# Optimization experiments

Measured on AMD Instinct MI355X. Metric: run time of the kernel, lower is better.

## Reference

```python
import jax, jax.numpy as jnp
import numpy as np

MAX_RADIUS = 3.0
NUM_BASIS = 8
NUM_NEIGHBORS = 16.0
N, E, NS, NV, B, D, T, L, HR = 2048, 32768, 32, 16, 8, 32, 32, 2, 64
NW = NS * 2 * NV + NV * 2 * (NS + NV) + NV * 2 * NV  # 3072 per-edge TP weights


def smooth_cutoff(x):
    u = 2.0 * (x - 1.0)
    y = 0.5 * (1.0 - jnp.cos(jnp.pi * u))
    y = jnp.where(u > 0, 0.0, y)
    y = jnp.where(u < -1, 1.0, y)
    return y


def bessel_basis(length):
    # soft_one_hot_linspace(basis='bessel', cutoff=False) * sqrt(NUM_BASIS)
    k = jnp.arange(1, NUM_BASIS + 1, dtype=length.dtype) * jnp.pi
    l = jnp.maximum(length, 1e-9)[..., None]
    return jnp.sqrt(2.0 / MAX_RADIUS) * jnp.sin(k * l / MAX_RADIUS) / l * np.sqrt(NUM_BASIS)


def get_edge_info(x, edge_src, edge_dst):
    n = x.shape[0]
    xr = x.reshape(n, 2, 3)                         # 2 vectors per node
    vec = xr[edge_src] - xr[edge_dst]               # [E,2,3]
    length = jnp.sqrt(jnp.sum(vec * vec, axis=-1) + 1e-12)   # [E,2]
    sh = np.sqrt(3.0) * vec / length[..., None]     # component-normalized l=1 SH
    feat = bessel_basis(length)                     # [E,2,B]
    attr = smooth_cutoff(length / MAX_RADIUS)[..., None] * sh  # [E,2,3]
    return feat.reshape(vec.shape[0], -1), attr


def setup_inputs() -> dict:
    key = jax.random.key(0)
    ks = jax.random.split(key, 20)
    inp = {
        'x': jax.random.normal(ks[0], (N, 6), jnp.float32),
        'batch': jnp.zeros((N,), jnp.int64 if jax.config.jax_enable_x64 else jnp.int32),
        'node_attr': jax.random.randint(ks[1], (N,), 0, T),
        'edge_src': jax.random.randint(ks[2], (E,), 0, N),
        'edge_dst': jax.random.randint(ks[3], (E,), 0, N),
        'emb': jax.random.normal(ks[4], (T, D), jnp.float32),
        'W_uplift': jax.random.normal(ks[5], (NV, 2), jnp.float32),
        'W_sc_s': jax.random.normal(ks[6], (L, NS, D, NS + NV), jnp.float32),
        'W_sc_v': jax.random.normal(ks[7], (L, NV, D, NV), jnp.float32),
        'W_l1_s': jax.random.normal(ks[8], (L, NS, NS), jnp.float32),
        'W_l1_v': jax.random.normal(ks[9], (L, NV, NV), jnp.float32),
        'W_r1': jax.random.normal(ks[10], (L, 2 * B, HR), jnp.float32),
        'W_r2': jax.random.normal(ks[11], (L, HR, NW), jnp.float32),
        'W_l2_s': jax.random.normal(ks[12], (L, NS + NV, NS + NV), jnp.float32),
        'W_l2_v': jax.random.normal(ks[13], (L, NV, NV), jnp.float32),
        'W_si_s': jax.random.normal(ks[14], (L, NS, NS), jnp.float32),
        'W_si_v': jax.random.normal(ks[15], (L, NV, NV), jnp.float32),
        'h': jnp.ones((L,), jnp.float32) * 0.01,
        'mix': jnp.ones((L,), jnp.float32) * 0.5,
    }
    return inp


def reference(x, batch, node_attr, edge_src, edge_dst, emb, W_uplift, W_sc_s, W_sc_v,
              W_l1_s, W_l1_v, W_r1, W_r2, W_l2_s, W_l2_v, W_si_s, W_si_v, h, mix):
    n = x.shape[0]
    a = emb[node_attr]                              # node attr embedding [N,D]
    Q, _ = jnp.linalg.qr(W_uplift)                  # semi-unitary uplift [NV,2]
    y_v = jnp.einsum('ci,nik->nck', Q, x.reshape(n, 2, 3))   # uplift vectors
    y_s = jnp.zeros((n, NS), x.dtype)
    y, y_old = (y_s, y_v), (y_s, y_v)
    n1 = NS * 2 * NV
    n2 = NV * 2 * (NS + NV)
    for i in range(L):
        ef, ea = get_edge_info(x, edge_src, edge_dst)       # [E,2B], [E,2,3]
        ys, yv = y
        # self-connection tensor product (features x node_attr)
        sc_s = jnp.einsum('ni,na,iaj->nj', ys, a, W_sc_s[i]) / np.sqrt(NS * D)
        sc_v = jnp.einsum('nck,na,caj->njk', yv, a, W_sc_v[i]) / np.sqrt(NV * D)
        # lin1
        s1 = ys @ W_l1_s[i] / np.sqrt(NS)
        v1 = jnp.einsum('nck,cj->njk', yv, W_l1_v[i]) / np.sqrt(NV)
        # radial MLP -> per-edge TP weights
        hr = jax.nn.silu(ef @ W_r1[i] / np.sqrt(2 * B))
        w = hr @ W_r2[i] / np.sqrt(HR)                       # [E,NW]
        w_sv = w[:, :n1].reshape(E, NS, 2, NV)
        w_vs = w[:, n1:n1 + n2].reshape(E, NV, 2, NS + NV)
        w_vv = w[:, n1 + n2:].reshape(E, NV, 2, NV)
        s_src, v_src = s1[edge_src], v1[edge_src]
        # edge tensor product: 0e x 1o -> 1o, 1o x 1o -> 0e (dot), 1o x 1o -> 1o (cross)
        e_v = jnp.einsum('esmj,es,emk->ejk', w_sv, s_src, ea) / np.sqrt(NS * 2)
        dots = jnp.einsum('eck,emk->ecm', v_src, ea)
        e_s = jnp.einsum('ecmj,ecm->ej', w_vs, dots) / np.sqrt(NV * 2 * 3)
        crs = jnp.cross(v_src[:, :, None, :], ea[:, None, :, :])  # [E,NV,2,3]
        e_v = e_v + jnp.einsum('ecmj,ecmk->ejk', w_vv, crs) / np.sqrt(NV * 2 * 2)
        # scatter-aggregate over destination nodes
        ns_ = jax.ops.segment_sum(e_s, edge_dst, num_segments=n) / np.sqrt(NUM_NEIGHBORS)
        nv_ = jax.ops.segment_sum(e_v, edge_dst, num_segments=n) / np.sqrt(NUM_NEIGHBORS)
        s2 = ns_ @ W_l2_s[i] / np.sqrt(NS + NV)
        v2 = jnp.einsum('nck,cj->njk', nv_, W_l2_v[i]) / np.sqrt(NV)
        conv_s, conv_v = sc_s + s2, sc_v + v2
        # gate
        g_s = jax.nn.silu(conv_s[:, :NS])
        g_v = jax.nn.sigmoid(conv_s[:, NS:])[:, :, None] * conv_v
        # self-interaction
        si_s = ys @ W_si_s[i] / np.sqrt(NS)
        si_v = jnp.einsum('nck,cj->njk', yv, W_si_v[i]) / np.sqrt(NV)
        # gated leapfrog update
        h2, m = h[i] ** 2, mix[i]
        new_s = 2 * ys - y_old[0] + h2 * (m * g_s + (m - 1) * si_s)
        new_v = 2 * yv - y_old[1] + h2 * (m * g_v + (m - 1) * si_v)
        y_old, y = y, (new_s, new_v)
        x = jnp.einsum('ci,nck->nik', Q, y[1]).reshape(n, 6)  # project back
    return x
```

## Files before the change

kernel.cpp:

```cpp
#include <hip/hip_runtime.h>
#include <hip/hip_bf16.h>
#include <math.h>

#define NN   2048
#define EE   32768
#define NS   32
#define NV   16
#define NB   8
#define DD   32
#define TT   32
#define LL   2
#define HRD  64
#define NWW  3072
#define TPE  128
#define PI_F 3.14159265358979323846f

#define SC_SCS (1.0f/32.0f)
#define SC_SCV 0.04419417382415922f
#define SC_L1S 0.17677669529663687f
#define SC_L1V 0.25f
#define SC_R1  0.25f
#define SC_R2  0.125f
#define SC_ES  0.10206207261596575f
#define SC_EV  0.125f
#define SC_AGG 0.25f
#define SC_L2S 0.14433756729740643f
#define SC_L2V 0.25f
#define SC_SIS 0.17677669529663687f
#define SC_SIV 0.25f

typedef __attribute__((ext_vector_type(8))) short  short8;
typedef __attribute__((ext_vector_type(4))) float  floatx4;

__device__ __forceinline__ floatx4 mfma16(short8 a, short8 b, floatx4 c) {
    return __builtin_amdgcn_mfma_f32_16x16x32_bf16(a, b, c, 0, 0, 0);
}

__device__ __forceinline__ void seg_reduce_store(
        const float (*red)[49], const int* dst_s,
        const int* __restrict__ row_ptr, int ebase,
        int tid, int wave, int lane,
        int* segstart_s, int* wtot_s, int* nseg_s,
        float* __restrict__ outg) {
    int seg_flag = 0, seg_lidx = 0;
    if (tid < TPE) {
        seg_flag = (tid == 0) || (dst_s[tid] != dst_s[tid - 1]);
        unsigned long long m = __ballot(seg_flag != 0);
        if (lane == 0) wtot_s[wave] = (int)__popcll(m);
        seg_lidx = (int)__popcll(m & ((1ull << lane) - 1ull));
    }
    __syncthreads();
    if (seg_flag) segstart_s[seg_lidx + (wave ? wtot_s[0] : 0)] = tid;
    if (tid == 0) {
        int ns = wtot_s[0] + wtot_s[1];
        nseg_s[0] = ns;
        segstart_s[ns] = TPE;
    }
    __syncthreads();
    int nseg = nseg_s[0];
    for (int w = tid; w < nseg * 48; w += 256) {
        int seg = w / 48, c = w - seg * 48;
        int p0 = segstart_s[seg], p1 = segstart_s[seg + 1];
        int d = dst_s[p0];
        float run = 0.f;
        for (int pos = p0; pos < p1; ++pos) run += red[pos][c];
        if (row_ptr[d] >= ebase && row_ptr[d + 1] <= ebase + TPE)
            outg[d * 48 + c] = run;
        else
            atomicAdd(&outg[d * 48 + c], run);
    }
}

__global__ void k_setup(const float* __restrict__ Wup, float* __restrict__ Q,
                        const float* __restrict__ emb,
                        const float* __restrict__ Wscs, const float* __restrict__ Wscv,
                        float* __restrict__ WtS, float* __restrict__ WtV,
                        const float* __restrict__ Wr2, __hip_bfloat16* __restrict__ wr2t,
                        int* __restrict__ deg, int* __restrict__ cursor) {
    int b = blockIdx.x;
    if (b == 0) {
        if (threadIdx.x != 0) return;
        double A[16][2], tau[2];
        for (int i = 0; i < 16; ++i)
            for (int j = 0; j < 2; ++j) A[i][j] = (double)Wup[i*2 + j];
        for (int j = 0; j < 2; ++j) {
            double alpha = A[j][j];
            double xn2 = 0.0;
            for (int i = j + 1; i < 16; ++i) xn2 += A[i][j]*A[i][j];
            if (xn2 == 0.0) {
                tau[j] = 0.0;
            } else {
                double nrm  = sqrt(alpha*alpha + xn2);
                double beta = (alpha >= 0.0) ? -nrm : nrm;
                tau[j] = (beta - alpha) / beta;
                double s = 1.0 / (alpha - beta);
                for (int i = j + 1; i < 16; ++i) A[i][j] *= s;
                A[j][j] = beta;
            }
            for (int k = j + 1; k < 2; ++k) {
                double w = A[j][k];
                for (int i = j + 1; i < 16; ++i) w += A[i][j]*A[i][k];
                w *= tau[j];
                A[j][k] -= w;
                for (int i = j + 1; i < 16; ++i) A[i][k] -= A[i][j]*w;
            }
        }
        double Qm[16][2];
        for (int i = 0; i < 16; ++i)
            for (int j = 0; j < 2; ++j) Qm[i][j] = (i == j) ? 1.0 : 0.0;
        for (int j = 1; j >= 0; --j) {
            for (int k = 0; k < 2; ++k) {
                double w = Qm[j][k];
                for (int i = j + 1; i < 16; ++i) w += A[i][j]*Qm[i][k];
                w *= tau[j];
                Qm[j][k] -= w;
                for (int i = j + 1; i < 16; ++i) Qm[i][k] -= A[i][j]*w;
            }
        }
        for (int i = 0; i < 16; ++i)
            for (int j = 0; j < 2; ++j) Q[i*2 + j] = (float)Qm[i][j];
    } else if (b <= 64) {
        int lt = b - 1;
        int l = lt >> 5, t = lt & 31;
        __shared__ float es[32];
        if (threadIdx.x < 32) es[threadIdx.x] = emb[t*DD + threadIdx.x];
        __syncthreads();
        const float* Ws = Wscs + (size_t)l*NS*DD*48;
        float* oS = WtS + (size_t)(l*TT + t)*NS*48;
        for (int idx = threadIdx.x; idx < NS*48; idx += 256) {
            int i = idx / 48, j = idx % 48;
            float acc = 0.f;
            for (int a = 0; a < 32; ++a) acc += es[a]*Ws[(i*DD + a)*48 + j];
            oS[idx] = acc;
        }
        const float* Wv = Wscv + (size_t)l*NV*DD*NV;
        float* oV = WtV + (size_t)(l*TT + t)*NV*NV;
        for (int idx = threadIdx.x; idx < NV*NV; idx += 256) {
            int c = idx / 16, j = idx % 16;
            float acc = 0.f;
            for (int a = 0; a < 32; ++a) acc += es[a]*Wv[(c*DD + a)*NV + j];
            oV[idx] = acc;
        }
    } else if (b <= 1600) {
        int idx = (b - 65)*256 + threadIdx.x;
        int l = idx / (HRD*NWW);
        int r = idx - l*(HRD*NWW);
        int k = r / NWW;
        int c = r - k*NWW;
        int ch = c >> 6, cc = c & 63, q = cc >> 4, tcc = cc & 15;
        int h = k >> 5, qd = (k >> 3) & 3, j = k & 7;
        size_t dst = (size_t)l*(NWW*HRD)
                   + (size_t)((ch*32 + q*8 + h*4 + qd)*128 + tcc*8 + j);
        wr2t[dst] = __float2bfloat16(Wr2[idx]);
    } else {
        int i = (b - 1601)*256 + threadIdx.x;
        if (i < NN) { deg[i] = 0; cursor[i] = 0; }
    }
}

__global__ void k_hist(const int* __restrict__ edst, int* __restrict__ deg) {
    int e = blockIdx.x*256 + threadIdx.x;
    atomicAdd(&deg[edst[e]], 1);
}

__global__ void k_scan(const int* __restrict__ deg, int* __restrict__ row_ptr) {
    __shared__ int wsum[4];
    int t = threadIdx.x;
    int lane = t & 63, wave = t >> 6;
    int loc[8]; int s = 0;
    for (int k = 0; k < 8; ++k) { loc[k] = deg[t*8 + k]; s += loc[k]; }
    int inc = s;
    for (int d = 1; d < 64; d <<= 1) {
        int v = __shfl_up(inc, d);
        if (lane >= d) inc += v;
    }
    if (lane == 63) wsum[wave] = inc;
    __syncthreads();
    int woff = 0;
    for (int w = 0; w < wave; ++w) woff += wsum[w];
    int off = woff + inc - s;
    for (int k = 0; k < 8; ++k) { row_ptr[t*8 + k] = off; off += loc[k]; }
    if (t == 255) row_ptr[2048] = off;
}

__global__ void k_fill(const int* __restrict__ esrc, const int* __restrict__ edst,
                       const int* __restrict__ row_ptr, int* __restrict__ cursor,
                       int* __restrict__ srcs, int* __restrict__ dsts,
                       const float* __restrict__ xin, const float* __restrict__ Q,
                       float* __restrict__ ys0, float* __restrict__ yv0,
                       float* __restrict__ ys1, float* __restrict__ yv1,
                       float* __restrict__ xcur,
                       const float* __restrict__ Wl1v0,
                       float* __restrict__ s1, float* __restrict__ v1,
                       float* __restrict__ nsb, float* __restrict__ nsb2,
                       float* __restrict__ nvba, float* __restrict__ nvbb) {
    if (blockIdx.x < 128) {
        int e = blockIdx.x*256 + threadIdx.x;
        int d = edst[e];
        int pos = atomicAdd(&cursor[d], 1);
        int p = row_ptr[d] + pos;
        srcs[p] = esrc[e];
        dsts[p] = d;
    } else {
        int idx = (blockIdx.x - 128)*256 + threadIdx.x;
        int n = idx / 48, r = idx - 48*(idx / 48);
        int j = r/3, k = r - 3*j;
        float xk  = xin[n*6 + k];
        float xk3 = xin[n*6 + 3 + k];
        float yvv = Q[j*2 + 0]*xk + Q[j*2 + 1]*xk3;
        yv0[idx] = yvv;
        yv1[idx] = yvv;
        float a = 0.f;
        for (int c = 0; c < 16; ++c) {
            float yc = Q[c*2 + 0]*xk + Q[c*2 + 1]*xk3;
            a += yc*Wl1v0[c*16 + j];
        }
        v1[idx] = a*SC_L1V;
        nsb[idx] = 0.f; nsb2[idx] = 0.f;
        nvba[idx] = 0.f; nvbb[idx] = 0.f;
        if (r < 32) {
            int si = n*32 + r;
            ys0[si] = 0.f; ys1[si] = 0.f; s1[si] = 0.f;
        }
        if (r < 6) xcur[n*6 + r] = xin[n*6 + r];
    }
}

__global__ void __launch_bounds__(256, 3) k_tp(
        const float* __restrict__ xcur,
        const int* __restrict__ srcs, const int* __restrict__ dsts,
        const int* __restrict__ row_ptr,
        const float* __restrict__ Wr1l,
        const __hip_bfloat16* __restrict__ wr2tl,
        const float* __restrict__ s1g, const float* __restrict__ v1g,
        float* __restrict__ nsb, float* __restrict__ nsb2,
        float* __restrict__ nvba, float* __restrict__ nvbb) {
    __shared__ __align__(16) char smem[31680];
    __shared__ float ea_s[TPE][9];
    __shared__ int   src_s[TPE];
    __shared__ int   dst_s[TPE];
    __shared__ int   segstart_s[TPE + 1];
    __shared__ int   wtot_s[2];
    __shared__ int   nseg_s[1];

    int bid = blockIdx.x;
    int region = bid % 3;
    int tile   = bid / 3;
    int ebase  = tile*TPE;
    int tid = threadIdx.x;
    int wave = tid >> 6, lane = tid & 63;
    int tc = tid & 15;
    int quad = lane >> 4;

    float* ef_lds  = (float*)smem;
    float* Wr1_lds = (float*)(smem + 8448);
    __hip_bfloat16* hr_lds = (__hip_bfloat16*)(smem + 12544);

    if (tid < TPE) { src_s[tid] = srcs[ebase + tid]; dst_s[tid] = dsts[ebase + tid]; }
    for (int i = tid; i < 16*64; i += 256) Wr1_lds[i] = Wr1l[i];

    if (tid < TPE) {
        int s = src_s[tid], d = dst_s[tid];
        for (int m = 0; m < 2; ++m) {
            float v0 = xcur[s*6 + m*3 + 0] - xcur[d*6 + m*3 + 0];
            float v1_ = xcur[s*6 + m*3 + 1] - xcur[d*6 + m*3 + 1];
            float v2 = xcur[s*6 + m*3 + 2] - xcur[d*6 + m*3 + 2];
            float len = sqrtf(v0*v0 + v1_*v1_ + v2*v2 + 1e-12f);
            float inv = 1.0f/len;
            float theta = len*(PI_F/3.0f);
            float s1v = sinf(theta), c1v = cosf(theta);
            float sc  = 2.3094010767585034f*inv;
            float sp = 0.f, scur = s1v, twoc = 2.f*c1v;
            for (int bq = 0; bq < 8; ++bq) {
                ef_lds[(m*8 + bq)*132 + tid] = sc*scur;
                float sn = twoc*scur - sp;
                sp = scur; scur = sn;
            }
            float u = 2.0f*(len*(1.0f/3.0f) - 1.0f);
            float cut;
            if (u > 0.f) cut = 0.f;
            else if (u < -1.f) cut = 1.f;
            else cut = 0.5f*(1.0f - cosf(PI_F*u));
            float shs = 1.7320508075688772f*inv*cut;
            ea_s[tid][m*3 + 0] = shs*v0;
            ea_s[tid][m*3 + 1] = shs*v1_;
            ea_s[tid][m*3 + 2] = shs*v2;
        }
    }
    __syncthreads();

    {
        int e = tid >> 1, h = tid & 1;
        float z[32];
        #pragma unroll
        for (int k = 0; k < 32; ++k) z[k] = 0.f;
        for (int f = 0; f < 16; ++f) {
            float efv = ef_lds[f*132 + e];
            #pragma unroll
            for (int k = 0; k < 32; ++k) z[k] += efv*Wr1_lds[f*64 + h*32 + k];
        }
        #pragma unroll
        for (int q8 = 0; q8 < 4; ++q8) {
            __hip_bfloat16 tmp[8];
            #pragma unroll
            for (int j = 0; j < 8; ++j) {
                float zz = z[q8*8 + j]*SC_R1;
                tmp[j] = __float2bfloat16(zz/(1.0f + expf(-zz)));
            }
            *(short8*)&hr_lds[e*72 + h*32 + q8*8] = *(short8*)tmp;
        }
    }
    __syncthreads();

    const short* hrp = (const short*)(smem + 12544);
    short8 a_lo[2], a_hi[2];
    #pragma unroll
    for (int rt = 0; rt < 2; ++rt) {
        int row = (wave*2 + rt)*16 + tc;
        a_lo[rt] = *(const short8*)(hrp + row*72 + quad*8);
        a_hi[rt] = *(const short8*)(hrp + row*72 + 32 + quad*8);
    }
    __syncthreads();

    const char* wb = (const char*)wr2tl;
    const float sES = SC_R2*SC_ES*SC_AGG;
    const float sEV = SC_R2*SC_EV*SC_AGG;

    if (region == 0) {
        float (*s1t)[132] = (float(*)[132])smem;
        for (int i = tid; i < TPE*32; i += 256) {
            int e = i >> 5, s = i & 31;
            s1t[s][e] = s1g[src_s[e]*32 + s];
        }
        __syncthreads();

        float accF[2][4][2] = {};
        for (int ci = 0; ci < 16; ++ci) {
            const char* Bc = wb + (size_t)ci*8192 + lane*16;
            #pragma unroll
            for (int q = 0; q < 4; ++q) {
                short8 b_lo = *(const short8*)(Bc + q*2048);
                short8 b_hi = *(const short8*)(Bc + q*2048 + 1024);
                floatx4 c0 = {0.f,0.f,0.f,0.f}, c1 = {0.f,0.f,0.f,0.f};
                c0 = mfma16(a_lo[0], b_lo, c0); c0 = mfma16(a_hi[0], b_hi, c0);
                c1 = mfma16(a_lo[1], b_lo, c1); c1 = mfma16(a_hi[1], b_hi, c1);
                int m = q & 1;
                int sidx = ci*2 + (q >> 1);
                #pragma unroll
                for (int rt = 0; rt < 2; ++rt) {
                    int e0r = (wave*2 + rt)*16 + quad*4;
                    float4 sv = *(const float4*)&s1t[sidx][e0r];
                    floatx4 cc = rt ? c1 : c0;
                    #pragma unroll
                    for (int i = 0; i < 4; ++i)
                        accF[rt][i][m] += cc[i]*((&sv.x)[i]);
                }
            }
        }
        __syncthreads();
        float (*red)[49] = (float(*)[49])smem;
        #pragma unroll
        for (int rt = 0; rt < 2; ++rt) {
            int e0r = (wave*2 + rt)*16 + quad*4;
            #pragma unroll
            for (int i = 0; i < 4; ++i) {
                int pos = e0r + i;
                float f0 = accF[rt][i][0]*sEV, f1 = accF[rt][i][1]*sEV;
                #pragma unroll
                for (int k = 0; k < 3; ++k)
                    red[pos][tc*3 + k] = f0*ea_s[pos][k] + f1*ea_s[pos][3 + k];
            }
        }
        __syncthreads();
        seg_reduce_store((const float(*)[49])smem, dst_s, row_ptr, ebase,
                         tid, wave, lane, segstart_s, wtot_s, nseg_s, nvba);
    } else if (region == 1) {
        float (*dots_t)[132] = (float(*)[132])smem;
        float (*v1h)[132]    = (float(*)[132])(smem + 16896);
        for (int half = 0; half < 2; ++half) {
            int jbase = half*24;
            for (int i = tid; i < TPE*24; i += 256) {
                int e = i/24, j = i - 24*(i/24);
                v1h[j][e] = v1g[src_s[e]*48 + jbase + j];
            }
            __syncthreads();
            for (int i = tid; i < TPE*16; i += 256) {
                int cm = i >> 7, e = i & (TPE - 1);
                int c = cm >> 1, m = cm & 1;
                dots_t[half*16 + cm][e] = v1h[c*3+0][e]*ea_s[e][m*3+0]
                                        + v1h[c*3+1][e]*ea_s[e][m*3+1]
                                        + v1h[c*3+2][e]*ea_s[e][m*3+2];
            }
            __syncthreads();
        }

        float accES[2][4][3] = {};
        for (int ci = 16; ci < 32; ++ci) {
            const char* Bc = wb + (size_t)ci*8192 + lane*16;
            #pragma unroll
            for (int q = 0; q < 4; ++q) {
                short8 b_lo = *(const short8*)(Bc + q*2048);
                short8 b_hi = *(const short8*)(Bc + q*2048 + 1024);
                floatx4 c0 = {0.f,0.f,0.f,0.f}, c1 = {0.f,0.f,0.f,0.f};
                c0 = mfma16(a_lo[0], b_lo, c0); c0 = mfma16(a_hi[0], b_hi, c0);
                c1 = mfma16(a_lo[1], b_lo, c1); c1 = mfma16(a_hi[1], b_hi, c1);
                int u = ci*4 + q - 64;
                int c = (u*10923) >> 16;
                int v6 = u - 6*c;
                int m = (v6 >= 3) ? 1 : 0;
                int g = v6 - 3*m;
                #pragma unroll
                for (int rt = 0; rt < 2; ++rt) {
                    int e0r = (wave*2 + rt)*16 + quad*4;
                    float4 dv = *(const float4*)&dots_t[c*2 + m][e0r];
                    floatx4 cc = rt ? c1 : c0;
                    #pragma unroll
                    for (int i = 0; i < 4; ++i)
                        accES[rt][i][g] += cc[i]*((&dv.x)[i]);
                }
            }
        }
        __syncthreads();
        float (*red)[49] = (float(*)[49])smem;
        #pragma unroll
        for (int rt = 0; rt < 2; ++rt) {
            int e0r = (wave*2 + rt)*16 + quad*4;
            #pragma unroll
            for (int i = 0; i < 4; ++i) {
                int pos = e0r + i;
                red[pos][tc]      = accES[rt][i][0]*sES;
                red[pos][16 + tc] = accES[rt][i][1]*sES;
                red[pos][32 + tc] = accES[rt][i][2]*sES;
            }
        }
        __syncthreads();
        seg_reduce_store((const float(*)[49])smem, dst_s, row_ptr, ebase,
                         tid, wave, lane, segstart_s, wtot_s, nseg_s, nsb);
    } else {
        float (*v1t)[132]  = (float(*)[132])smem;
        float (*dots2)[132] = (float(*)[132])(smem + 25344);
        for (int i = tid; i < TPE*48; i += 256) {
            int e = i/48, j = i%48;
            v1t[j][e] = v1g[src_s[e]*48 + j];
        }
        __syncthreads();
        for (int i = tid; i < 12*TPE; i += 256) {
            int r = i >> 7, e = i & (TPE - 1);
            int c = 10 + (r >> 1), m = r & 1;
            dots2[r][e] = v1t[c*3+0][e]*ea_s[e][m*3+0]
                        + v1t[c*3+1][e]*ea_s[e][m*3+1]
                        + v1t[c*3+2][e]*ea_s[e][m*3+2];
        }
        __syncthreads();

        float accES[2][4][3] = {};
        float accV[2][4][2][3] = {};
        for (int ci = 32; ci < 48; ++ci) {
            const char* Bc = wb + (size_t)ci*8192 + lane*16;
            #pragma unroll
            for (int q = 0; q < 4; ++q) {
                short8 b_lo = *(const short8*)(Bc + q*2048);
                short8 b_hi = *(const short8*)(Bc + q*2048 + 1024);
                floatx4 c0 = {0.f,0.f,0.f,0.f}, c1 = {0.f,0.f,0.f,0.f};
                c0 = mfma16(a_lo[0], b_lo, c0); c0 = mfma16(a_hi[0], b_hi, c0);
                c1 = mfma16(a_lo[1], b_lo, c1); c1 = mfma16(a_hi[1], b_hi, c1);
                if (ci < 40) {
                    int u = ci*4 + q - 64;
                    int c = (u*10923) >> 16;
                    int v6 = u - 6*c;
                    int m = (v6 >= 3) ? 1 : 0;
                    int g = v6 - 3*m;
                    int dr = (c - 10)*2 + m;
                    #pragma unroll
                    for (int rt = 0; rt < 2; ++rt) {
                        int e0r = (wave*2 + rt)*16 + quad*4;
                        float4 dv = *(const float4*)&dots2[dr][e0r];
                        floatx4 cc = rt ? c1 : c0;
                        #pragma unroll
                        for (int i = 0; i < 4; ++i)
                            accES[rt][i][g] += cc[i]*((&dv.x)[i]);
                    }
                } else {
                    int c = ci*2 - 80 + (q >> 1);
                    int m = q & 1;
                    #pragma unroll
                    for (int rt = 0; rt < 2; ++rt) {
                        int e0r = (wave*2 + rt)*16 + quad*4;
                        float4 vx = *(const float4*)&v1t[c*3 + 0][e0r];
                        float4 vy = *(const float4*)&v1t[c*3 + 1][e0r];
                        float4 vz = *(const float4*)&v1t[c*3 + 2][e0r];
                        floatx4 cc = rt ? c1 : c0;
                        #pragma unroll
                        for (int i = 0; i < 4; ++i) {
                            float ww = cc[i];
                            accV[rt][i][m][0] += ww*((&vx.x)[i]);
                            accV[rt][i][m][1] += ww*((&vy.x)[i]);
                            accV[rt][i][m][2] += ww*((&vz.x)[i]);
                        }
                    }
                }
            }
        }
        __syncthreads();
        float (*red)[49] = (float(*)[49])smem;
        #pragma unroll
        for (int rt = 0; rt < 2; ++rt) {
            int e0r = (wave*2 + rt)*16 + quad*4;
            #pragma unroll
            for (int i = 0; i < 4; ++i) {
                int pos = e0r + i;
                red[pos][tc]      = accES[rt][i][0]*sES;
                red[pos][16 + tc] = accES[rt][i][1]*sES;
                red[pos][32 + tc] = accES[rt][i][2]*sES;
            }
        }
        __syncthreads();
        seg_reduce_store((const float(*)[49])smem, dst_s, row_ptr, ebase,
                         tid, wave, lane, segstart_s, wtot_s, nseg_s, nsb2);
        __syncthreads();
        #pragma unroll
        for (int rt = 0; rt < 2; ++rt) {
            int e0r = (wave*2 + rt)*16 + quad*4;
            #pragma unroll
            for (int i = 0; i < 4; ++i) {
                int pos = e0r + i;
                float u00 = accV[rt][i][0][0], u01 = accV[rt][i][0][1], u02 = accV[rt][i][0][2];
                float u10 = accV[rt][i][1][0], u11 = accV[rt][i][1][1], u12 = accV[rt][i][1][2];
                float a0 = ea_s[pos][0], a1 = ea_s[pos][1], a2 = ea_s[pos][2];
                float b0 = ea_s[pos][3], b1 = ea_s[pos][4], b2 = ea_s[pos][5];
                red[pos][tc*3 + 0] = (u01*a2 - u02*a1 + u11*b2 - u12*b1)*sEV;
                red[pos][tc*3 + 1] = (u02*a0 - u00*a2 + u12*b0 - u10*b2)*sEV;
                red[pos][tc*3 + 2] = (u00*a1 - u01*a0 + u10*b1 - u11*b0)*sEV;
            }
        }
        __syncthreads();
        seg_reduce_store((const float(*)[49])smem, dst_s, row_ptr, ebase,
                         tid, wave, lane, segstart_s, wtot_s, nseg_s, nvbb);
    }
}

__global__ void __launch_bounds__(256) k_nodepost(
        const float* __restrict__ ysC, const float* __restrict__ yvC,
        float* __restrict__ ysO, float* __restrict__ yvO,
        const float* __restrict__ nsb, const float* __restrict__ nsb2,
        const float* __restrict__ nvba, const float* __restrict__ nvbb,
        const int* __restrict__ nattr,
        const float* __restrict__ WtSl, const float* __restrict__ WtVl,
        const float* __restrict__ Wl2s, const float* __restrict__ Wl2v,
        const float* __restrict__ Wsis, const float* __restrict__ Wsiv,
        const float* __restrict__ harr, const float* __restrict__ mixarr, int l,
        float* __restrict__ xcur, float* __restrict__ xout2,
        const float* __restrict__ Qg,
        const float* __restrict__ Wl1sN, const float* __restrict__ Wl1vN,
        float* __restrict__ s1, float* __restrict__ v1,
        float* __restrict__ znsb, float* __restrict__ znsb2,
        float* __restrict__ znvba, float* __restrict__ znvbb,
        int do_next) {
    int wave = threadIdx.x >> 6, lane = threadIdx.x & 63;
    int n = blockIdx.x*4 + wave;
    __shared__ float ys_s[4][32], yv_s[4][48], ns_s[4][48], nv_s[4][48];
    __shared__ float cs_s[4][48], nvo_s[4][48], nsn_s[4][32];

    if (lane < 32) ys_s[wave][lane] = ysC[n*32 + lane];
    if (lane < 48) {
        yv_s[wave][lane] = yvC[n*48 + lane];
        ns_s[wave][lane] = nsb[n*48 + lane] + nsb2[n*48 + lane];
        nv_s[wave][lane] = nvba[n*48 + lane] + nvbb[n*48 + lane];
    }
    __syncthreads();
    int t = nattr[n];
    const float* WtSn = WtSl + (size_t)t*NS*48;
    const float* WtVn = WtVl + (size_t)t*NV*NV;
    float hv = harr[l];
    float h2 = hv*hv, mx = mixarr[l];

    if (lane < 48) {
        float sc = 0.f, s2 = 0.f;
        for (int i = 0; i < 32; ++i) sc += ys_s[wave][i]*WtSn[i*48 + lane];
        for (int c = 0; c < 48; ++c) s2 += ns_s[wave][c]*Wl2s[c*48 + lane];
        cs_s[wave][lane] = sc*SC_SCS + s2*SC_L2S;
    }
    __syncthreads();
    if (lane < 48) {
        int j = lane/3, k = lane - 3*j;
        float scv = 0.f, v2 = 0.f, siv = 0.f;
        for (int c = 0; c < 16; ++c) {
            float yvv = yv_s[wave][c*3 + k];
            scv += yvv*WtVn[c*16 + j];
            v2  += nv_s[wave][c*3 + k]*Wl2v[c*16 + j];
            siv += yvv*Wsiv[c*16 + j];
        }
        float convv = scv*SC_SCV + v2*SC_L2V;
        siv *= SC_SIV;
        float gate = 1.f/(1.f + expf(-cs_s[wave][32 + j]));
        float gv = gate*convv;
        float nvnew = 2.f*yv_s[wave][lane] - yvO[n*48 + lane] + h2*(mx*gv + (mx - 1.f)*siv);
        nvo_s[wave][lane] = nvnew;
        yvO[n*48 + lane] = nvnew;
    }
    if (lane < 32) {
        float sis = 0.f;
        for (int i = 0; i < 32; ++i) sis += ys_s[wave][i]*Wsis[i*32 + lane];
        sis *= SC_SIS;
        float cs = cs_s[wave][lane];
        float gs = cs/(1.f + expf(-cs));
        float nsnew = 2.f*ys_s[wave][lane] - ysO[n*32 + lane] + h2*(mx*gs + (mx - 1.f)*sis);
        nsn_s[wave][lane] = nsnew;
        ysO[n*32 + lane] = nsnew;
    }
    __syncthreads();
    if (lane < 6) {
        int i = lane/3, k = lane - 3*(lane/3);
        float acc = 0.f;
        for (int c = 0; c < 16; ++c) acc += Qg[c*2 + i]*nvo_s[wave][c*3 + k];
        xcur[n*6 + lane]  = acc;
        xout2[n*6 + lane] = acc;
    }
    if (do_next) {
        if (lane < 32) {
            float a = 0.f;
            for (int i = 0; i < 32; ++i) a += nsn_s[wave][i]*Wl1sN[i*32 + lane];
            s1[n*32 + lane] = a*SC_L1S;
        }
        if (lane < 48) {
            int j = lane/3, k = lane - 3*j;
            float a = 0.f;
            for (int c = 0; c < 16; ++c) a += nvo_s[wave][c*3 + k]*Wl1vN[c*16 + j];
            v1[n*48 + lane] = a*SC_L1V;
            znsb[n*48 + lane] = 0.f; znsb2[n*48 + lane] = 0.f;
            znvba[n*48 + lane] = 0.f; znvbb[n*48 + lane] = 0.f;
        }
    }
}

extern "C" void kernel_launch(void* const* d_in, const int* in_sizes, int n_in,
                              void* d_out, int out_size, void* d_ws, size_t ws_size,
                              hipStream_t stream) {
    const float* x_in  = (const float*)d_in[0];
    const int*   nattr = (const int*)  d_in[2];
    const int*   esrc  = (const int*)  d_in[3];
    const int*   edst  = (const int*)  d_in[4];
    const float* emb   = (const float*)d_in[5];
    const float* Wup   = (const float*)d_in[6];
    const float* Wscs  = (const float*)d_in[7];
    const float* Wscv  = (const float*)d_in[8];
    const float* Wl1s  = (const float*)d_in[9];
    const float* Wl1v  = (const float*)d_in[10];
    const float* Wr1   = (const float*)d_in[11];
    const float* Wr2   = (const float*)d_in[12];
    const float* Wl2s  = (const float*)d_in[13];
    const float* Wl2v  = (const float*)d_in[14];
    const float* Wsis  = (const float*)d_in[15];
    const float* Wsiv  = (const float*)d_in[16];
    const float* harr  = (const float*)d_in[17];
    const float* mixar = (const float*)d_in[18];
    float* out = (float*)d_out;

    float* ws = (float*)d_ws;
    size_t off = 0;
    float* Q    = ws + off; off += 32;
    float* WtS  = ws + off; off += (size_t)LL*TT*NS*48;
    float* WtV  = ws + off; off += (size_t)LL*TT*NV*NV;
    float* ys0  = ws + off; off += (size_t)NN*32;
    float* yv0  = ws + off; off += (size_t)NN*48;
    float* ys1  = ws + off; off += (size_t)NN*32;
    float* yv1  = ws + off; off += (size_t)NN*48;
    float* xcur = ws + off; off += (size_t)NN*6;
    float* s1   = ws + off; off += (size_t)NN*32;
    float* v1   = ws + off; off += (size_t)NN*48;
    float* nsb  = ws + off; off += (size_t)NN*48;
    float* nsb2 = ws + off; off += (size_t)NN*48;
    float* nvba = ws + off; off += (size_t)NN*48;
    float* nvbb = ws + off; off += (size_t)NN*48;
    off = (off + 3) & ~(size_t)3;
    __hip_bfloat16* wr2t = (__hip_bfloat16*)(ws + off); off += (size_t)LL*NWW*HRD/2;
    int* deg     = (int*)(ws + off); off += NN;
    int* cursor  = (int*)(ws + off); off += NN;
    int* row_ptr = (int*)(ws + off); off += NN + 1;
    int* srcs    = (int*)(ws + off); off += EE;
    int* dsts    = (int*)(ws + off); off += EE;

    k_setup<<<1609, 256, 0, stream>>>(Wup, Q, emb, Wscs, Wscv, WtS, WtV, Wr2, wr2t,
                                      deg, cursor);
    k_hist<<<EE/256, 256, 0, stream>>>(edst, deg);
    k_scan<<<1, 256, 0, stream>>>(deg, row_ptr);
    k_fill<<<128 + NN*48/256, 256, 0, stream>>>(esrc, edst, row_ptr, cursor, srcs, dsts,
                                    x_in, Q, ys0, yv0, ys1, yv1, xcur,
                                    Wl1v, s1, v1, nsb, nsb2, nvba, nvbb);

    float* curS = ys0; float* curV = yv0;
    float* oldS = ys1; float* oldV = yv1;
    for (int l = 0; l < LL; ++l) {
        k_tp<<<3*EE/TPE, 256, 0, stream>>>(xcur, srcs, dsts, row_ptr,
                                           Wr1 + (size_t)l*16*64,
                                           wr2t + (size_t)l*NWW*HRD,
                                           s1, v1, nsb, nsb2, nvba, nvbb);
        float* xo2 = (l == LL - 1) ? out : xcur;
        int lN = (l + 1 < LL) ? (l + 1) : l;
        k_nodepost<<<NN/4, 256, 0, stream>>>(curS, curV, oldS, oldV,
                                             nsb, nsb2, nvba, nvbb, nattr,
                                             WtS + (size_t)l*TT*NS*48, WtV + (size_t)l*TT*NV*NV,
                                             Wl2s + (size_t)l*48*48, Wl2v + (size_t)l*16*16,
                                             Wsis + (size_t)l*32*32, Wsiv + (size_t)l*16*16,
                                             harr, mixar, l, xcur, xo2, Q,
                                             Wl1s + (size_t)lN*32*32, Wl1v + (size_t)lN*16*16,
                                             s1, v1, nsb, nsb2, nvba, nvbb,
                                             (l + 1 < LL) ? 1 : 0);
        float* ts = curS; curS = oldS; oldS = ts;
        float* tv = curV; curV = oldV; oldV = tv;
    }
}
```

Measured before the change: 231.7 us.

## Double-buffer TP weight chunks in LDS via async global-to-LDS loads

The per-edge TP weight (wr2) B-fragments are now staged into a double-buffered LDS region with global_load_lds, prefetching the next chunk while MFMAs run on the current one, instead of each wave loading directly from global memory. Region 2 also drops its precomputed dots2 table and recomputes the v1·ea dot products inline from v1t and ea_s, which frees LDS for the staging buffer. LDS per block grows to hold the buffers, which may reduce occupancy under launch_bounds(256,3). Each chunk iteration also adds a barrier.

After: 231.6 us. Within noise of the previous version (-0.0%).

```diff
diff --git a/kernel.cpp b/kernel.cpp
--- a/kernel.cpp
+++ b/kernel.cpp
@@ -31,6 +31,12 @@
 
 typedef __attribute__((ext_vector_type(8))) short  short8;
 typedef __attribute__((ext_vector_type(4))) float  floatx4;
+
+__device__ __forceinline__ void load_lds16(const void* g, void* l) {
+    __builtin_amdgcn_global_load_lds(
+        (const __attribute__((address_space(1))) unsigned int*)g,
+        (__attribute__((address_space(3))) unsigned int*)l, 16, 0, 0);
+}
 
 __device__ __forceinline__ floatx4 mfma16(short8 a, short8 b, floatx4 c) {
     return __builtin_amdgcn_mfma_f32_16x16x32_bf16(a, b, c, 0, 0, 0);
@@ -235,7 +241,7 @@
         const float* __restrict__ s1g, const float* __restrict__ v1g,
         float* __restrict__ nsb, float* __restrict__ nsb2,
         float* __restrict__ nvba, float* __restrict__ nvbb) {
-    __shared__ __align__(16) char smem[31680];
+    __shared__ __align__(16) char smem[41728];
     __shared__ float ea_s[TPE][9];
     __shared__ int   src_s[TPE];
     __shared__ int   dst_s[TPE];
@@ -326,21 +332,35 @@
     const float sES = SC_R2*SC_ES*SC_AGG;
     const float sEV = SC_R2*SC_EV*SC_AGG;
 
+    char* Bbuf;
+    if (region == 0)      Bbuf = smem + 16896;
+    else if (region == 1) Bbuf = smem + 16896;
+    else                  Bbuf = smem + 25344;
+
+    auto stage = [&](int ch, int b) {
+        const char* g = wb + (size_t)ch*8192 + wave*2048 + lane*16;
+        char* l = Bbuf + b*8192 + wave*2048;
+        load_lds16(g, l);
+        load_lds16(g + 1024, l + 1024);
+    };
+
     if (region == 0) {
         float (*s1t)[132] = (float(*)[132])smem;
         for (int i = tid; i < TPE*32; i += 256) {
             int e = i >> 5, s = i & 31;
             s1t[s][e] = s1g[src_s[e]*32 + s];
         }
-        __syncthreads();
+        stage(0, 0);
 
         float accF[2][4][2] = {};
         for (int ci = 0; ci < 16; ++ci) {
-            const char* Bc = wb + (size_t)ci*8192 + lane*16;
+            __syncthreads();
+            if (ci + 1 < 16) stage(ci + 1, (ci + 1) & 1);
+            const char* B = Bbuf + (ci & 1)*8192;
             #pragma unroll
             for (int q = 0; q < 4; ++q) {
-                short8 b_lo = *(const short8*)(Bc + q*2048);
-                short8 b_hi = *(const short8*)(Bc + q*2048 + 1024);
+                short8 b_lo = *(const short8*)(B + (q*8 + quad)*256 + tc*16);
+                short8 b_hi = *(const short8*)(B + (q*8 + 4 + quad)*256 + tc*16);
                 floatx4 c0 = {0.f,0.f,0.f,0.f}, c1 = {0.f,0.f,0.f,0.f};
                 c0 = mfma16(a_lo[0], b_lo, c0); c0 = mfma16(a_hi[0], b_hi, c0);
                 c1 = mfma16(a_lo[1], b_lo, c1); c1 = mfma16(a_hi[1], b_hi, c1);
@@ -393,14 +413,17 @@
             }
             __syncthreads();
         }
+        stage(16, 0);
 
         float accES[2][4][3] = {};
         for (int ci = 16; ci < 32; ++ci) {
-            const char* Bc = wb + (size_t)ci*8192 + lane*16;
+            __syncthreads();
+            if (ci + 1 < 32) stage(ci + 1, (ci + 1) & 1);
+            const char* B = Bbuf + (ci & 1)*8192;
             #pragma unroll
             for (int q = 0; q < 4; ++q) {
-                short8 b_lo = *(const short8*)(Bc + q*2048);
-                short8 b_hi = *(const short8*)(Bc + q*2048 + 1024);
+                short8 b_lo = *(const short8*)(B + (q*8 + quad)*256 + tc*16);
+                short8 b_hi = *(const short8*)(B + (q*8 + 4 + quad)*256 + tc*16);
                 floatx4 c0 = {0.f,0.f,0.f,0.f}, c1 = {0.f,0.f,0.f,0.f};
                 c0 = mfma16(a_lo[0], b_lo, c0); c0 = mfma16(a_hi[0], b_hi, c0);
                 c1 = mfma16(a_lo[1], b_lo, c1); c1 = mfma16(a_hi[1], b_hi, c1);
@@ -437,30 +460,23 @@
         seg_reduce_store((const float(*)[49])smem, dst_s, row_ptr, ebase,
                          tid, wave, lane, segstart_s, wtot_s, nseg_s, nsb);
     } else {
-        float (*v1t)[132]  = (float(*)[132])smem;
-        float (*dots2)[132] = (float(*)[132])(smem + 25344);
+        float (*v1t)[132] = (float(*)[132])smem;
         for (int i = tid; i < TPE*48; i += 256) {
             int e = i/48, j = i%48;
             v1t[j][e] = v1g[src_s[e]*48 + j];
         }
-        __syncthreads();
-        for (int i = tid; i < 12*TPE; i += 256) {
-            int r = i >> 7, e = i & (TPE - 1);
-            int c = 10 + (r >> 1), m = r & 1;
-            dots2[r][e] = v1t[c*3+0][e]*ea_s[e][m*3+0]
-                        + v1t[c*3+1][e]*ea_s[e][m*3+1]
-                        + v1t[c*3+2][e]*ea_s[e][m*3+2];
-        }
-        __syncthreads();
+        stage(32, 0);
 
         float accES[2][4][3] = {};
         float accV[2][4][2][3] = {};
         for (int ci = 32; ci < 48; ++ci) {
-            const char* Bc = wb + (size_t)ci*8192 + lane*16;
+            __syncthreads();
+            if (ci + 1 < 48) stage(ci + 1, (ci + 1) & 1);
+            const char* B = Bbuf + (ci & 1)*8192;
             #pragma unroll
             for (int q = 0; q < 4; ++q) {
-                short8 b_lo = *(const short8*)(Bc + q*2048);
-                short8 b_hi = *(const short8*)(Bc + q*2048 + 1024);
+                short8 b_lo = *(const short8*)(B + (q*8 + quad)*256 + tc*16);
+                short8 b_hi = *(const short8*)(B + (q*8 + 4 + quad)*256 + tc*16);
                 floatx4 c0 = {0.f,0.f,0.f,0.f}, c1 = {0.f,0.f,0.f,0.f};
                 c0 = mfma16(a_lo[0], b_lo, c0); c0 = mfma16(a_hi[0], b_hi, c0);
                 c1 = mfma16(a_lo[1], b_lo, c1); c1 = mfma16(a_hi[1], b_hi, c1);
@@ -470,15 +486,20 @@
                     int v6 = u - 6*c;
                     int m = (v6 >= 3) ? 1 : 0;
                     int g = v6 - 3*m;
-                    int dr = (c - 10)*2 + m;
                     #pragma unroll
                     for (int rt = 0; rt < 2; ++rt) {
                         int e0r = (wave*2 + rt)*16 + quad*4;
-                        float4 dv = *(const float4*)&dots2[dr][e0r];
+                        float4 vx = *(const float4*)&v1t[c*3 + 0][e0r];
+                        float4 vy = *(const float4*)&v1t[c*3 + 1][e0r];
+                        float4 vz = *(const float4*)&v1t[c*3 + 2][e0r];
                         floatx4 cc = rt ? c1 : c0;
                         #pragma unroll
-                        for (int i = 0; i < 4; ++i)
-                            accES[rt][i][g] += cc[i]*((&dv.x)[i]);
+                        for (int i = 0; i < 4; ++i) {
+                            float dot = (&vx.x)[i]*ea_s[e0r + i][m*3 + 0]
+                                      + (&vy.x)[i]*ea_s[e0r + i][m*3 + 1]
+                                      + (&vz.x)[i]*ea_s[e0r + i][m*3 + 2];
+                            accES[rt][i][g] += cc[i]*dot;
+                        }
                     }
                 } else {
                     int c = ci*2 - 80 + (q >> 1);
```
